# Kernel tuning notes

Measured on AMD Instinct MI355X. Metric: run time of the kernel, lower is better.

## Reference

```python
import jax, jax.numpy as jnp
import numpy as np

N, E, IN_DIM, HID, HEADS, OUT_DIM, T = 50000, 200000, 32, 64, 4, 32, 3
NEG_SLOPE = 0.2  # PyG GATv2Conv default


def setup_inputs() -> dict:
    key = jax.random.key(0)
    ks = jax.random.split(key, 16)
    s = 0.1
    return {
        "feat": jax.random.normal(ks[0], (N, IN_DIM), jnp.float32),
        "W_in": jax.random.normal(ks[1], (IN_DIM, HID), jnp.float32) * s,
        "b_in": jnp.zeros((HID,), jnp.float32),
        "Wl": jax.random.normal(ks[2], (2 * HID, HEADS * HID), jnp.float32) * s,
        "bl": jnp.zeros((HEADS * HID,), jnp.float32),
        "Wr": jax.random.normal(ks[3], (2 * HID, HEADS * HID), jnp.float32) * s,
        "br": jnp.zeros((HEADS * HID,), jnp.float32),
        "att": jax.random.normal(ks[4], (HEADS, HID), jnp.float32) * s,
        "b_conv": jnp.zeros((HEADS * HID,), jnp.float32),
        "Wg": jax.random.normal(ks[5], (HID, OUT_DIM), jnp.float32) * s,
        "bg": jnp.zeros((OUT_DIM,), jnp.float32),
        "edge_index": jax.random.randint(ks[6], (2, E), 0, N, jnp.int32),
        "node_mask": jax.random.randint(ks[7], (N,), 0, T + 1, jnp.int32),
        "current_state": jax.random.randint(ks[8], (N,), 0, 2, jnp.int32),
    }


def reference(feat, W_in, b_in, Wl, bl, Wr, br, att, b_conv, Wg, bg,
              edge_index, node_mask, current_state):
    # add self loops (GATv2Conv add_self_loops=True)
    loops = jnp.arange(N, dtype=edge_index.dtype)
    src = jnp.concatenate([edge_index[0], loops])  # [E+N]
    dst = jnp.concatenate([edge_index[1], loops])

    h0 = feat @ W_in + b_in  # [N, HID]
    bias_sum = b_conv.reshape(HEADS, HID).sum(0)  # heads are summed after bias add

    def step(h, i):
        active = node_mask > i  # [N] bool: nodes updated at this step
        x = jnp.concatenate([h, h0], axis=-1)  # [N, 2*HID]
        xl = (x @ Wl + bl).reshape(N, HEADS, HID)  # source transform
        xr = (x @ Wr + br).reshape(N, HEADS, HID)  # target transform
        e_act = active[src] & active[dst]  # edge alive iff both endpoints active
        s = jax.nn.leaky_relu(xl[src] + xr[dst], NEG_SLOPE)  # [E+N, H, C]
        score = jnp.einsum('ehc,hc->eh', s, att)  # [E+N, H]
        score = jnp.where(e_act[:, None], score, -1e30)
        smax = jax.lax.stop_gradient(
            jax.ops.segment_max(score, dst, num_segments=N))  # [N, H]
        ex = jnp.exp(score - smax[dst]) * e_act[:, None].astype(score.dtype)
        denom = jax.ops.segment_sum(ex, dst, num_segments=N)  # [N, H]
        alpha = ex / jnp.maximum(denom[dst], 1e-16)  # segment softmax per dst
        msg = alpha[:, :, None] * xl[src]  # [E+N, H, C]
        agg = jax.ops.segment_sum(msg, dst, num_segments=N)  # [N, H, C]
        out = jnp.tanh(agg.sum(1) + bias_sum)  # sum over heads, then Tanh
        return jnp.where(active[:, None], out, h), None

    h, _ = jax.lax.scan(step, h0, jnp.arange(T))
    # original returns g_embed(h[current_state]); fixed-shape variant: mask rows
    out = (h @ Wg + bg) * (current_state[:, None] > 0).astype(h.dtype)
    return out
```

## Files before the change

### kernel.cpp

```cpp
#include <hip/hip_runtime.h>
#include <hip/hip_bf16.h>

#define NN      50000
#define EE      200000
#define IN_DIM  32
#define HID     64
#define HEADS   4
#define OUTD    32
#define TSTEPS  3

typedef unsigned short bf16_t;
typedef __attribute__((ext_vector_type(8))) short  short8;
typedef __attribute__((ext_vector_type(4))) float  floatx4;

__device__ __forceinline__ float b2f(bf16_t u) {
    union { unsigned int i; float f; } v; v.i = ((unsigned int)u) << 16; return v.f;
}
__device__ __forceinline__ bf16_t f2b(float f) {
    union { float f; unsigned int i; } v; v.f = f;
    unsigned int r = v.i + 0x7FFF + ((v.i >> 16) & 1);
    return (bf16_t)(r >> 16);
}

#define DPP_ADD(x, ctrl) ((x) + __int_as_float(                                 \
        __builtin_amdgcn_update_dpp(0, __float_as_int(x), (ctrl), 0xF, 0xF, true)))

#define H0_BLOCKS ((NN + 31) / 32)
#define NB_NODE   ((NN + 255) / 256)
#define NBC       (NB_NODE * 4)

__global__ __launch_bounds__(256) void k_setup(
        const void* W_in, const void* b_in, const void* att, const void* bconv,
        const void* Wg, const void* bg,
        const void* Wl_raw, const void* Wr_raw, const void* bl_raw, const void* br_raw,
        const void* feat_raw, const int* __restrict__ nmask,
        float* attf, float* bcf, float* Wgf, float* bgf,
        bf16_t* __restrict__ Wt, bf16_t* __restrict__ WtS, float* __restrict__ bb,
        int* __restrict__ deg, int* __restrict__ flag, int* __restrict__ bcount,
        bf16_t* __restrict__ h0, bf16_t* __restrict__ h) {
    __shared__ int bad;
    __shared__ float Ws[IN_DIM * HID];
    __shared__ float bs[HID];
    __shared__ int wcnt[4][4];
    int t = threadIdx.x, bid = blockIdx.x;
    if (t == 0) bad = 0;
    __syncthreads();
    {
        const bf16_t* p = (const bf16_t*)W_in;
        int mybad = 0;
        for (int i = t; i < IN_DIM * HID; i += 256) {
            float v = b2f(p[i]);
            if (v != v || fabsf(v) > 100.f) mybad = 1;
        }
        if (mybad) atomicOr(&bad, 1);
    }
    __syncthreads();
    int f = bad ? 0 : 1;
    if (bid == 0 && t == 0) *flag = f;

    if (bid < 256) {
        int i = bid * 256 + t;
        int n = i >> 7, k = i & 127;
        const void* W = (n < 256) ? Wl_raw : Wr_raw;
        int nn = (n < 256) ? n : n - 256;
        float v = f ? b2f(((const bf16_t*)W)[k * 256 + nn])
                    : ((const float*)W)[k * 256 + nn];
        Wt[n * 128 + k] = f2b(v);
        if (k < 64) {
            float v2 = f ? b2f(((const bf16_t*)W)[(k + 64) * 256 + nn])
                         : ((const float*)W)[(k + 64) * 256 + nn];
            WtS[n * 64 + k] = f2b(v + v2);
        }
        if (k == 0) {
            const void* b = (n < 256) ? bl_raw : br_raw;
            bb[n] = f ? b2f(((const bf16_t*)b)[nn]) : ((const float*)b)[nn];
        }
    } else if (bid < 267) {
        int i = (bid - 256) * 256 + t;
        const void* src; float* dst; int off;
        if      (i < 256)  { src = att;   dst = attf; off = i; }
        else if (i < 512)  { src = bconv; dst = bcf;  off = i - 256; }
        else if (i < 2560) { src = Wg;    dst = Wgf;  off = i - 512; }
        else if (i < 2592) { src = bg;    dst = bgf;  off = i - 2560; }
        else return;
        dst[off] = f ? b2f(((const bf16_t*)src)[off]) : ((const float*)src)[off];
    } else if (bid < 267 + NB_NODE) {
        int nb = bid - 267;
        int i = nb * 256 + t;
        bool valid = i < NN;
        if (valid) deg[i] = 0;
        int wid = t >> 6, lane = t & 63;
        int v = 0;
        if (valid) { int m = nmask[i]; v = m < 0 ? 0 : (m > 3 ? 3 : m); }
#pragma unroll
        for (int b = 0; b < 4; b++) {
            unsigned long long mm = __ballot(valid && v == b);
            if (lane == 0) wcnt[wid][b] = __popcll(mm);
        }
        __syncthreads();
        if (t < 4)
            bcount[nb * 4 + t] = wcnt[0][t] + wcnt[1][t] + wcnt[2][t] + wcnt[3][t];
    } else {
        for (int i = t; i < IN_DIM * HID; i += 256)
            Ws[i] = f ? b2f(((const bf16_t*)W_in)[i]) : ((const float*)W_in)[i];
        if (t < HID)
            bs[t] = f ? b2f(((const bf16_t*)b_in)[t]) : ((const float*)b_in)[t];
        __syncthreads();
        int nb = bid - (267 + NB_NODE);
        int wid = t >> 6, c = t & 63;
#pragma unroll
        for (int g = 0; g < 8; g++) {
            int node = (nb * 8 + g) * 4 + wid;
            if (node >= NN) break;
            float acc = bs[c];
            if (f) {
                const short8* fr8 = (const short8*)((const bf16_t*)feat_raw
                                                    + (size_t)node * IN_DIM);
#pragma unroll
                for (int j = 0; j < 4; j++) {
                    short8 fv = fr8[j];
#pragma unroll
                    for (int k = 0; k < 8; k++)
                        acc += b2f((bf16_t)fv[k]) * Ws[(j * 8 + k) * HID + c];
                }
            } else {
                const float4* fr4 = (const float4*)((const float*)feat_raw
                                                    + (size_t)node * IN_DIM);
#pragma unroll
                for (int j = 0; j < 8; j++) {
                    float4 fv = fr4[j];
                    acc += fv.x * Ws[(j * 4 + 0) * HID + c];
                    acc += fv.y * Ws[(j * 4 + 1) * HID + c];
                    acc += fv.z * Ws[(j * 4 + 2) * HID + c];
                    acc += fv.w * Ws[(j * 4 + 3) * HID + c];
                }
            }
            bf16_t o = f2b(acc);
            h0[(size_t)node * HID + c] = o;
            h [(size_t)node * HID + c] = o;
        }
    }
}

__global__ __launch_bounds__(256) void k_hist(const int* __restrict__ dst,
                                              int* __restrict__ deg) {
    int i = (blockIdx.x * 256 + threadIdx.x) * 4;
    if (i + 3 < EE) {
        int4 d = *(const int4*)(dst + i);
        atomicAdd(&deg[d.x], 1);
        atomicAdd(&deg[d.y], 1);
        atomicAdd(&deg[d.z], 1);
        atomicAdd(&deg[d.w], 1);
    } else {
        for (; i < EE; i++) atomicAdd(&deg[dst[i]], 1);
    }
}

__global__ __launch_bounds__(256) void k_scan(const int* __restrict__ deg,
                                              int* __restrict__ row_ptr,
                                              int* __restrict__ cursor,
                                              const int* __restrict__ bcount,
                                              int* __restrict__ mbuf,
                                              int n, int nch) {
    __shared__ int sc[256];
    __shared__ int spre[256];
    __shared__ int cb[4];
    int t = threadIdx.x, bid = blockIdx.x;

    if (bid == 0) {
        if (t < 4) cb[t] = 0;
        __syncthreads();
        for (int i = t; i < NBC; i += 256) atomicAdd(&cb[i & 3], bcount[i]);
        __syncthreads();
        if (t == 0) {
            int c1 = cb[1], c2 = cb[2], c3 = cb[3];
            mbuf[7] = 0;
            mbuf[6] = c3;
            mbuf[5] = c3 + c2;
            mbuf[4] = c3 + c2 + c1;
            mbuf[8] = c3 + c2 + c1;
            mbuf[9] = c3 + c2;
            mbuf[10] = c3;
        }
    }

    int base = bid * 1024;
    int pre = 0;
    {
        const int4* d4 = (const int4*)deg;
        int lim = base >> 2;
        for (int i = t; i < lim; i += 256) {
            int4 q = d4[i];
            pre += q.x + q.y + q.z + q.w;
        }
    }
    spre[t] = pre; __syncthreads();
    for (int off = 128; off > 0; off >>= 1) {
        if (t < off) spre[t] += spre[t + off];
        __syncthreads();
    }
    int bpref = spre[0];

    int v[4]; int s = 0;
#pragma unroll
    for (int j = 0; j < 4; j++) {
        int i = base + t * 4 + j;
        v[j] = (i < n) ? deg[i] : 0;
        s += v[j];
    }
    sc[t] = s; __syncthreads();
    for (int off = 1; off < 256; off <<= 1) {
        int add = (t >= off) ? sc[t - off] : 0;
        __syncthreads();
        sc[t] += add;
        __syncthreads();
    }
    int run = sc[t] - s + bpref;
#pragma unroll
    for (int j = 0; j < 4; j++) {
        int i = base + t * 4 + j;
        if (i < n) { row_ptr[i] = run; cursor[i] = run; }
        run += v[j];
    }
    if (bid == nch - 1 && t == 255) row_ptr[n] = run;
}

__global__ __launch_bounds__(256) void k_scatter_all(const int* __restrict__ src,
                                                     const int* __restrict__ dst,
                                                     int* __restrict__ cursor,
                                                     int* __restrict__ col,
                                                     const int* __restrict__ mask,
                                                     int* __restrict__ mbuf,
                                                     int* __restrict__ order) {
    int t = threadIdx.x, bid = blockIdx.x;
    int i = bid * 256 + t;
    if (i < EE) {
        int sv = src[i];
        int m = mask[sv]; m = m < 0 ? 0 : (m > 3 ? 3 : m);
        int d = dst[i];
        int pos = atomicAdd(&cursor[d], 1);
        col[pos] = sv | (m << 28);
    }
    if (bid < NB_NODE) {
        __shared__ int wcnt[4][4];
        __shared__ int bbase[4];
        int wid = t >> 6, lane = t & 63;
        int ni = bid * 256 + t;
        bool valid = ni < NN;
        int v = 0;
        if (valid) { int m = mask[ni]; v = m < 0 ? 0 : (m > 3 ? 3 : m); }
        int rank = 0;
#pragma unroll
        for (int b = 0; b < 4; b++) {
            unsigned long long mm = __ballot(valid && v == b);
            if (valid && v == b)
                rank = __popcll(mm & ((lane == 0) ? 0ull : (~0ull >> (64 - lane))));
            if (lane == 0) wcnt[wid][b] = __popcll(mm);
        }
        __syncthreads();
        if (t < 4) {
            int tot = wcnt[0][t] + wcnt[1][t] + wcnt[2][t] + wcnt[3][t];
            bbase[t] = atomicAdd(&mbuf[4 + t], tot);
        }
        __syncthreads();
        if (valid) {
            int wpre = 0;
            for (int ww = 0; ww < wid; ww++) wpre += wcnt[ww][v];
            order[bbase[v] + wpre + rank] = ni;
        }
    }
}

__global__ __launch_bounds__(256) void k_gemm0(const bf16_t* __restrict__ h0,
                                               const bf16_t* __restrict__ WtS,
                                               const float* __restrict__ bb,
                                               bf16_t* __restrict__ xl,
                                               bf16_t* __restrict__ xr,
                                               const int* __restrict__ order,
                                               const int* __restrict__ mbuf) {
    int count = mbuf[8];
    int mbase = blockIdx.x * 64;
    if (mbase >= count) return;

    __shared__ bf16_t smem[64 * 72 + 128 * 72];
    bf16_t* As = smem;
    bf16_t* Bs = smem + 64 * 72;
    bf16_t* Cs = smem;

    int t = threadIdx.x;
    int nbase = blockIdx.y * 128;

    {
        int ln = t >> 2, lq = t & 3;
        int idx = mbase + ln;
        int node = (idx < count) ? order[idx] : -1;
        ulonglong2 z; z.x = 0; z.y = 0;
        ulonglong2 v0 = z, v1 = z;
        if (node >= 0) {
            v0 = *(const ulonglong2*)(h0 + (size_t)node * HID + lq * 16);
            v1 = *(const ulonglong2*)(h0 + (size_t)node * HID + lq * 16 + 8);
        }
        *(ulonglong2*)(&As[ln * 72 + lq * 16]) = v0;
        *(ulonglong2*)(&As[ln * 72 + lq * 16 + 8]) = v1;
    }
    {
        int n = t >> 1, kc = (t & 1) * 32;
        const bf16_t* srcp = WtS + (size_t)(nbase + n) * 64 + kc;
        bf16_t* dstp = &Bs[n * 72 + kc];
        *(ulonglong2*)(dstp)      = *(const ulonglong2*)(srcp);
        *(ulonglong2*)(dstp + 8)  = *(const ulonglong2*)(srcp + 8);
        *(ulonglong2*)(dstp + 16) = *(const ulonglong2*)(srcp + 16);
        *(ulonglong2*)(dstp + 24) = *(const ulonglong2*)(srcp + 24);
    }
    __syncthreads();

    int wv = t >> 6, lane = t & 63, mrow = lane & 15, quad = lane >> 4;
    floatx4 acc[8];
#pragma unroll
    for (int nf = 0; nf < 8; nf++) acc[nf] = (floatx4){0.f, 0.f, 0.f, 0.f};
#pragma unroll
    for (int kq = 0; kq < 2; kq++) {
        short8 a = *(const short8*)(&As[(wv * 16 + mrow) * 72 + kq * 32 + quad * 8]);
#pragma unroll
        for (int nf = 0; nf < 8; nf++) {
            short8 b = *(const short8*)(&Bs[(nf * 16 + mrow) * 72 + kq * 32 + quad * 8]);
            acc[nf] = __builtin_amdgcn_mfma_f32_16x16x32_bf16(a, b, acc[nf], 0, 0, 0);
        }
    }
    __syncthreads();

#pragma unroll
    for (int nf = 0; nf < 8; nf++) {
        float bv = bb[nbase + nf * 16 + mrow];
#pragma unroll
        for (int r = 0; r < 4; r++) {
            int m = wv * 16 + quad * 4 + r;
            Cs[m * 136 + nf * 16 + mrow] = f2b(acc[nf][r] + bv);
        }
    }
    __syncthreads();

    bf16_t* outp = (blockIdx.y < 2) ? xl : xr;
    int cc = (blockIdx.y & 1) * 128;
#pragma unroll
    for (int i = 0; i < 4; i++) {
        int c = t + i * 256;
        int m = c >> 4, kc = (c & 15) * 8;
        int idx = mbase + m;
        if (idx < count) {
            int node = order[idx];
            *(ulonglong2*)(outp + (size_t)node * 256 + cc + kc) =
                *(const ulonglong2*)(&Cs[m * 136 + kc]);
        }
    }
}

__global__ __launch_bounds__(256) void k_gemm_mfma(const bf16_t* __restrict__ h,
                                                   const bf16_t* __restrict__ h0,
                                                   const bf16_t* __restrict__ Wt,
                                                   const float* __restrict__ bb,
                                                   bf16_t* __restrict__ xl,
                                                   bf16_t* __restrict__ xr,
                                                   const int* __restrict__ order,
                                                   const int* __restrict__ mbuf,
                                                   int step) {
    int count = mbuf[8 + step];
    int mbase = blockIdx.x * 64;
    if (mbase >= count) return;

    __shared__ bf16_t smem[64 * 136 + 128 * 136];
    bf16_t* As = smem;
    bf16_t* Bs = smem + 64 * 136;
    bf16_t* Cs = smem;

    int t = threadIdx.x;
    int nbase = blockIdx.y * 128;

    {
        int ln = t >> 2, lq = t & 3;
        int idx = mbase + ln;
        int node = (idx < count) ? order[idx] : -1;
        ulonglong2 z; z.x = 0; z.y = 0;
#pragma unroll
        for (int j = 0; j < 2; j++) {
            int chunk = lq + j * 4;
            ulonglong2 vh = z, vh0 = z;
            if (node >= 0) {
                vh  = *(const ulonglong2*)(h  + (size_t)node * HID + chunk * 8);
                vh0 = *(const ulonglong2*)(h0 + (size_t)node * HID + chunk * 8);
            }
            *(ulonglong2*)(&As[ln * 136 + chunk * 8]) = vh;
            *(ulonglong2*)(&As[ln * 136 + 64 + chunk * 8]) = vh0;
        }
    }
#pragma unroll
    for (int i = 0; i < 8; i++) {
        int c = t + i * 256;
        int n = c >> 4, kc = (c & 15) * 8;
        *(ulonglong2*)(&Bs[n * 136 + kc]) =
            *(const ulonglong2*)(Wt + (size_t)(nbase + n) * 128 + kc);
    }
    __syncthreads();

    int wv = t >> 6, lane = t & 63, mrow = lane & 15, quad = lane >> 4;
    floatx4 acc[8];
#pragma unroll
    for (int nf = 0; nf < 8; nf++) acc[nf] = (floatx4){0.f, 0.f, 0.f, 0.f};
#pragma unroll
    for (int kq = 0; kq < 4; kq++) {
        short8 a = *(const short8*)(&As[(wv * 16 + mrow) * 136 + kq * 32 + quad * 8]);
#pragma unroll
        for (int nf = 0; nf < 8; nf++) {
            short8 b = *(const short8*)(&Bs[(nf * 16 + mrow) * 136 + kq * 32 + quad * 8]);
            acc[nf] = __builtin_amdgcn_mfma_f32_16x16x32_bf16(a, b, acc[nf], 0, 0, 0);
        }
    }
    __syncthreads();

#pragma unroll
    for (int nf = 0; nf < 8; nf++) {
        float bv = bb[nbase + nf * 16 + mrow];
#pragma unroll
        for (int r = 0; r < 4; r++) {
            int m = wv * 16 + quad * 4 + r;
            Cs[m * 136 + nf * 16 + mrow] = f2b(acc[nf][r] + bv);
        }
    }
    __syncthreads();

    bf16_t* outp = (blockIdx.y < 2) ? xl : xr;
    int cc = (blockIdx.y & 1) * 128;
#pragma unroll
    for (int i = 0; i < 4; i++) {
        int c = t + i * 256;
        int m = c >> 4, kc = (c & 15) * 8;
        int idx = mbase + m;
        if (idx < count) {
            int node = order[idx];
            *(ulonglong2*)(outp + (size_t)node * 256 + cc + kc) =
                *(const ulonglong2*)(&Cs[m * 136 + kc]);
        }
    }
}

__global__ __launch_bounds__(256) void k_agg(bf16_t* __restrict__ h,
                                             const bf16_t* __restrict__ xl,
                                             const bf16_t* __restrict__ xr,
                                             const float* __restrict__ att,
                                             const float* __restrict__ b_conv,
                                             const int* __restrict__ row_ptr,
                                             const int* __restrict__ col,
                                             const int* __restrict__ order,
                                             const int* __restrict__ mbuf,
                                             int step) {
    int count = mbuf[8 + step];
    int wid = threadIdx.x >> 6;
    int lane = threadIdx.x & 63;
    float4 attv = *(const float4*)(att + lane * 4);
    float4 bcv  = *(const float4*)(b_conv + lane * 4);

    for (int idx = blockIdx.x * 4 + wid; idx < count; idx += gridDim.x * 4) {
        int node = order[idx];

        ushort4 xru = *(const ushort4*)(xr + (size_t)node * 256 + lane * 4);
        float xr0 = b2f(xru.x), xr1 = b2f(xru.y), xr2 = b2f(xru.z), xr3 = b2f(xru.w);

        float a0 = 0.f, a1 = 0.f, a2 = 0.f, a3 = 0.f, l = 0.f;

        auto ld = [&](int s) {
            return *(const ushort4*)(xl + (size_t)s * 256 + lane * 4);
        };
        auto body = [&](ushort4 xu) {
            float x0 = b2f(xu.x), x1 = b2f(xu.y), x2 = b2f(xu.z), x3 = b2f(xu.w);
            float v0 = x0 + xr0; v0 = v0 > 0.f ? v0 : 0.2f * v0;
            float v1 = x1 + xr1; v1 = v1 > 0.f ? v1 : 0.2f * v1;
            float v2 = x2 + xr2; v2 = v2 > 0.f ? v2 : 0.2f * v2;
            float v3 = x3 + xr3; v3 = v3 > 0.f ? v3 : 0.2f * v3;
            float part = attv.x * v0 + attv.y * v1 + attv.z * v2 + attv.w * v3;
            part = DPP_ADD(part, 0xB1);
            part = DPP_ADD(part, 0x4E);
            part = DPP_ADD(part, 0x141);
            part = DPP_ADD(part, 0x140);
            float p = __expf(part);
            l += p;
            a0 += p * x0; a1 += p * x1; a2 += p * x2; a3 += p * x3;
        };

        int q0 = node, q1 = 0, q2 = 0, q3 = 0;
        int qn = 1;
        int e0 = row_ptr[node], e1 = row_ptr[node + 1];
        for (int e = e0; e < e1; e++) {
            int c = col[e];
            if (((unsigned)c >> 28) > (unsigned)step) {
                int s = c & 0x0FFFFFFF;
                if (qn == 0) q0 = s;
                else if (qn == 1) q1 = s;
                else if (qn == 2) q2 = s;
                else q3 = s;
                if (++qn == 4) {
                    ushort4 u0 = ld(q0), u1 = ld(q1), u2 = ld(q2), u3 = ld(q3);
                    body(u0); body(u1); body(u2); body(u3);
                    qn = 0;
                }
            }
        }
        if (qn) {
            ushort4 u0 = ld(q0), u1, u2;
            if (qn > 1) u1 = ld(q1);
            if (qn > 2) u2 = ld(q2);
            body(u0);
            if (qn > 1) body(u1);
            if (qn > 2) body(u2);
        }

        float inv = 1.f / l;
        float t0 = a0 * inv + bcv.x;
        float t1 = a1 * inv + bcv.y;
        float t2 = a2 * inv + bcv.z;
        float t3 = a3 * inv + bcv.w;
        t0 += __shfl_xor(t0, 16, 64); t0 += __shfl_xor(t0, 32, 64);
        t1 += __shfl_xor(t1, 16, 64); t1 += __shfl_xor(t1, 32, 64);
        t2 += __shfl_xor(t2, 16, 64); t2 += __shfl_xor(t2, 32, 64);
        t3 += __shfl_xor(t3, 16, 64); t3 += __shfl_xor(t3, 32, 64);
        if (lane < 16) {
            ushort4 o;
            o.x = f2b(tanhf(t0)); o.y = f2b(tanhf(t1));
            o.z = f2b(tanhf(t2)); o.w = f2b(tanhf(t3));
            *(ushort4*)(h + (size_t)node * HID + lane * 4) = o;
        }
    }
}

__global__ __launch_bounds__(256) void k_out(const bf16_t* __restrict__ h,
                                             const float* __restrict__ Wg,
                                             const float* __restrict__ bg,
                                             const int* __restrict__ cs,
                                             void* __restrict__ out,
                                             const int* __restrict__ flag) {
    __shared__ float Ws[HID * OUTD];
    __shared__ float bs[OUTD];
    int t = threadIdx.x;
    for (int i = t; i < HID * OUTD; i += 256) Ws[i] = Wg[i];
    if (t < OUTD) bs[t] = bg[t];
    __syncthreads();
    int node = blockIdx.x * 8 + (t >> 5);
    int c = t & 31;
    if (node >= NN) return;
    float res = 0.f;
    if (cs[node] > 0) {
        const short8* hr8 = (const short8*)(h + (size_t)node * HID);
        float acc = bs[c];
#pragma unroll
        for (int j = 0; j < 8; j++) {
            short8 hv = hr8[j];
#pragma unroll
            for (int k = 0; k < 8; k++)
                acc += b2f((bf16_t)hv[k]) * Ws[(j * 8 + k) * OUTD + c];
        }
        res = acc;
    }
    size_t idx = (size_t)node * OUTD + c;
    if (*flag) ((bf16_t*)out)[idx] = f2b(res);
    else       ((float*)out)[idx]  = res;
}

static inline size_t alignup(size_t x) { return (x + 255) & ~(size_t)255; }

extern "C" void kernel_launch(void* const* d_in, const int* in_sizes, int n_in,
                              void* d_out, int out_size, void* d_ws, size_t ws_size,
                              hipStream_t stream) {
    const void* feat_raw  = d_in[0];
    const void* W_in_raw  = d_in[1];
    const void* b_in_raw  = d_in[2];
    const void* Wl_raw    = d_in[3];
    const void* bl_raw    = d_in[4];
    const void* Wr_raw    = d_in[5];
    const void* br_raw    = d_in[6];
    const void* att_raw   = d_in[7];
    const void* bconv_raw = d_in[8];
    const void* Wg_raw    = d_in[9];
    const void* bg_raw    = d_in[10];
    const int* edge       = (const int*)d_in[11];
    const int* nmask      = (const int*)d_in[12];
    const int* cstate     = (const int*)d_in[13];

    const int* e_src = edge;
    const int* e_dst = edge + EE;

    const size_t SZ_HB   = alignup((size_t)NN * HID * sizeof(bf16_t));
    const size_t SZ_X    = alignup((size_t)NN * 256 * sizeof(bf16_t));
    const size_t SZ_I    = alignup((size_t)NN * sizeof(int));
    const size_t SZ_RP   = alignup((size_t)(NN + 1) * sizeof(int));
    const size_t SZ_COL  = alignup((size_t)EE * sizeof(int));
    const int nch = (NN + 1023) / 1024;
    const size_t SZ_BC   = alignup((size_t)NBC * sizeof(int));
    const size_t SZ_WT   = alignup((size_t)512 * 128 * sizeof(bf16_t));
    const size_t SZ_WTS  = alignup((size_t)512 * 64 * sizeof(bf16_t));
    const size_t SZ_B    = alignup(512 * sizeof(float));
    const size_t SZ_WG   = alignup((size_t)HID * OUTD * sizeof(float));

    char* w = (char*)d_ws;
    bf16_t* h0   = (bf16_t*)w; w += SZ_HB;
    bf16_t* h    = (bf16_t*)w; w += SZ_HB;
    bf16_t* xl   = (bf16_t*)w; w += SZ_X;
    bf16_t* xr   = (bf16_t*)w; w += SZ_X;
    int* deg     = (int*)w;    w += SZ_I;
    int* row_ptr = (int*)w;    w += SZ_RP;
    int* cursor  = (int*)w;    w += SZ_I;
    int* colA    = (int*)w;    w += SZ_COL;
    int* order   = (int*)w;    w += SZ_I;
    int* bcount  = (int*)w;    w += SZ_BC;
    bf16_t* Wt   = (bf16_t*)w; w += SZ_WT;
    bf16_t* WtS  = (bf16_t*)w; w += SZ_WTS;
    float* bb    = (float*)w;  w += SZ_B;
    float* attf  = (float*)w;  w += SZ_B;
    float* bcf   = (float*)w;  w += SZ_B;
    float* Wgf   = (float*)w;  w += SZ_WG;
    float* bgf   = (float*)w;  w += SZ_B;
    int* flag    = (int*)w;    w += 256;
    int* mbuf    = (int*)w;    w += 256;
    if ((size_t)(w - (char*)d_ws) > ws_size) return;

    k_setup<<<467 + H0_BLOCKS - 4, 256, 0, stream>>>(
        W_in_raw, b_in_raw, att_raw, bconv_raw, Wg_raw, bg_raw,
        Wl_raw, Wr_raw, bl_raw, br_raw, feat_raw, nmask,
        attf, bcf, Wgf, bgf, Wt, WtS, bb, deg, flag, bcount, h0, h);

    k_hist<<<(EE + 1023) / 1024, 256, 0, stream>>>(e_dst, deg);
    k_scan<<<nch, 256, 0, stream>>>(deg, row_ptr, cursor, bcount, mbuf, NN, nch);
    k_scatter_all<<<(EE + 255) / 256, 256, 0, stream>>>(e_src, e_dst, cursor, colA,
                                                        nmask, mbuf, order);

    k_gemm0<<<dim3((NN + 63) / 64, 4), 256, 0, stream>>>(h0, WtS, bb, xl, xr, order, mbuf);
    k_agg<<<2048, 256, 0, stream>>>(h, xl, xr, attf, bcf, row_ptr, colA, order, mbuf, 0);

    for (int s = 1; s < TSTEPS; s++) {
        k_gemm_mfma<<<dim3((NN + 63) / 64, 4), 256, 0, stream>>>(h, h0, Wt, bb, xl, xr,
                                                                 order, mbuf, s);
        k_agg<<<2048, 256, 0, stream>>>(h, xl, xr, attf, bcf,
                                        row_ptr, colA, order, mbuf, s);
    }

    k_out<<<(NN + 7) / 8, 256, 0, stream>>>(h, Wgf, bgf, cstate, d_out, flag);
}
```

Baseline: 275.3 us.

## Bucket CSR edges by source mask level and add dynamic work-stealing aggregation

```diff
diff --git a/kernel.cpp b/kernel.cpp
--- a/kernel.cpp
+++ b/kernel.cpp
@@ -25,18 +25,20 @@
 #define DPP_ADD(x, ctrl) ((x) + __int_as_float(                                 \
         __builtin_amdgcn_update_dpp(0, __float_as_int(x), (ctrl), 0xF, 0xF, true)))
 
-#define H0_BLOCKS ((NN + 31) / 32)
+#define H0_BLOCKS ((NN + 63) / 64)
 #define NB_NODE   ((NN + 255) / 256)
 #define NBC       (NB_NODE * 4)
+#define EB        ((EE + 1023) / 1024)
 
 __global__ __launch_bounds__(256) void k_setup(
         const void* W_in, const void* b_in, const void* att, const void* bconv,
         const void* Wg, const void* bg,
         const void* Wl_raw, const void* Wr_raw, const void* bl_raw, const void* br_raw,
         const void* feat_raw, const int* __restrict__ nmask,
+        const int* __restrict__ e_src, const int* __restrict__ e_dst,
         float* attf, float* bcf, float* Wgf, float* bgf,
         bf16_t* __restrict__ Wt, bf16_t* __restrict__ WtS, float* __restrict__ bb,
-        int* __restrict__ deg, int* __restrict__ flag, int* __restrict__ bcount,
+        int* __restrict__ deg4, int* __restrict__ flag, int* __restrict__ bcount,
         bf16_t* __restrict__ h0, bf16_t* __restrict__ h) {
     __shared__ int bad;
     __shared__ float Ws[IN_DIM * HID];
@@ -88,7 +90,6 @@
         int nb = bid - 267;
         int i = nb * 256 + t;
         bool valid = i < NN;
-        if (valid) deg[i] = 0;
         int wid = t >> 6, lane = t & 63;
         int v = 0;
         if (valid) { int m = nmask[i]; v = m < 0 ? 0 : (m > 3 ? 3 : m); }
@@ -100,17 +101,38 @@
         __syncthreads();
         if (t < 4)
             bcount[nb * 4 + t] = wcnt[0][t] + wcnt[1][t] + wcnt[2][t] + wcnt[3][t];
+    } else if (bid < 267 + NB_NODE + EB) {
+        int nb = bid - 267 - NB_NODE;
+        int i = (nb * 256 + t) * 4;
+        if (i + 3 < EE) {
+            int4 dv = *(const int4*)(e_dst + i);
+            int4 sv = *(const int4*)(e_src + i);
+            int m0 = nmask[sv.x]; m0 = m0 < 0 ? 0 : (m0 > 3 ? 3 : m0);
+            int m1 = nmask[sv.y]; m1 = m1 < 0 ? 0 : (m1 > 3 ? 3 : m1);
+            int m2 = nmask[sv.z]; m2 = m2 < 0 ? 0 : (m2 > 3 ? 3 : m2);
+            int m3 = nmask[sv.w]; m3 = m3 < 0 ? 0 : (m3 > 3 ? 3 : m3);
+            atomicAdd(&deg4[dv.x * 4 + m0], 1);
+            atomicAdd(&deg4[dv.y * 4 + m1], 1);
+            atomicAdd(&deg4[dv.z * 4 + m2], 1);
+            atomicAdd(&deg4[dv.w * 4 + m3], 1);
+        } else {
+            for (; i < EE; i++) {
+                int s = e_src[i];
+                int m = nmask[s]; m = m < 0 ? 0 : (m > 3 ? 3 : m);
+                atomicAdd(&deg4[e_dst[i] * 4 + m], 1);
+            }
+        }
     } else {
         for (int i = t; i < IN_DIM * HID; i += 256)
             Ws[i] = f ? b2f(((const bf16_t*)W_in)[i]) : ((const float*)W_in)[i];
         if (t < HID)
             bs[t] = f ? b2f(((const bf16_t*)b_in)[t]) : ((const float*)b_in)[t];
         __syncthreads();
-        int nb = bid - (267 + NB_NODE);
+        int nb = bid - (267 + NB_NODE + EB);
         int wid = t >> 6, c = t & 63;
 #pragma unroll
-        for (int g = 0; g < 8; g++) {
-            int node = (nb * 8 + g) * 4 + wid;
+        for (int g = 0; g < 16; g++) {
+            int node = (nb * 16 + g) * 4 + wid;
             if (node >= NN) break;
             float acc = bs[c];
             if (f) {
@@ -142,23 +164,9 @@
     }
 }
 
-__global__ __launch_bounds__(256) void k_hist(const int* __restrict__ dst,
-                                              int* __restrict__ deg) {
-    int i = (blockIdx.x * 256 + threadIdx.x) * 4;
-    if (i + 3 < EE) {
-        int4 d = *(const int4*)(dst + i);
-        atomicAdd(&deg[d.x], 1);
-        atomicAdd(&deg[d.y], 1);
-        atomicAdd(&deg[d.z], 1);
-        atomicAdd(&deg[d.w], 1);
-    } else {
-        for (; i < EE; i++) atomicAdd(&deg[dst[i]], 1);
-    }
-}
-
-__global__ __launch_bounds__(256) void k_scan(const int* __restrict__ deg,
-                                              int* __restrict__ row_ptr,
-                                              int* __restrict__ cursor,
+__global__ __launch_bounds__(256) void k_scan(const int* __restrict__ deg4,
+                                              int* __restrict__ cur4,
+                                              int* __restrict__ rend4,
                                               const int* __restrict__ bcount,
                                               int* __restrict__ mbuf,
                                               int n, int nch) {
@@ -184,15 +192,12 @@
         }
     }
 
+    const int4* d4 = (const int4*)deg4;
     int base = bid * 1024;
     int pre = 0;
-    {
-        const int4* d4 = (const int4*)deg;
-        int lim = base >> 2;
-        for (int i = t; i < lim; i += 256) {
-            int4 q = d4[i];
-            pre += q.x + q.y + q.z + q.w;
-        }
+    for (int i = t; i < base; i += 256) {
+        int4 q = d4[i];
+        pre += q.x + q.y + q.z + q.w;
     }
     spre[t] = pre; __syncthreads();
     for (int off = 128; off > 0; off >>= 1) {
@@ -201,12 +206,14 @@
     }
     int bpref = spre[0];
 
-    int v[4]; int s = 0;
+    int4 dd[4]; int tot[4]; int s = 0;
 #pragma unroll
     for (int j = 0; j < 4; j++) {
         int i = base + t * 4 + j;
-        v[j] = (i < n) ? deg[i] : 0;
-        s += v[j];
+        if (i < n) dd[j] = d4[i];
+        else { dd[j].x = 0; dd[j].y = 0; dd[j].z = 0; dd[j].w = 0; }
+        tot[j] = dd[j].x + dd[j].y + dd[j].z + dd[j].w;
+        s += tot[j];
     }
     sc[t] = s; __syncthreads();
     for (int off = 1; off < 256; off <<= 1) {
@@ -219,15 +226,23 @@
 #pragma unroll
     for (int j = 0; j < 4; j++) {
         int i = base + t * 4 + j;
-        if (i < n) { row_ptr[i] = run; cursor[i] = run; }
-        run += v[j];
-    }
-    if (bid == nch - 1 && t == 255) row_ptr[n] = run;
+        if (i < n) {
+            int c3 = run;
+            int c2 = c3 + dd[j].w;
+            int c1 = c2 + dd[j].z;
+            int c0 = c1 + dd[j].y;
+            int4 cu; cu.x = c0; cu.y = c1; cu.z = c2; cu.w = c3;
+            *(int4*)(cur4 + i * 4) = cu;
+            int4 re; re.x = c0; re.y = c1; re.z = c2; re.w = run;
+            *(int4*)(rend4 + i * 4) = re;
+        }
+        run += tot[j];
+    }
 }
 
 __global__ __launch_bounds__(256) void k_scatter_all(const int* __restrict__ src,
                                                      const int* __restrict__ dst,
-                                                     int* __restrict__ cursor,
+                                                     int* __restrict__ cur4,
                                                      int* __restrict__ col,
                                                      const int* __restrict__ mask,
                                                      int* __restrict__ mbuf,
@@ -238,8 +253,8 @@
         int sv = src[i];
         int m = mask[sv]; m = m < 0 ? 0 : (m > 3 ? 3 : m);
         int d = dst[i];
-        int pos = atomicAdd(&cursor[d], 1);
-        col[pos] = sv | (m << 28);
+        int pos = atomicAdd(&cur4[d * 4 + m], 1);
+        col[pos] = sv;
     }
     if (bid < NB_NODE) {
         __shared__ int wcnt[4][4];
@@ -448,85 +463,94 @@
                                              const bf16_t* __restrict__ xr,
                                              const float* __restrict__ att,
                                              const float* __restrict__ b_conv,
-                                             const int* __restrict__ row_ptr,
+                                             const int* __restrict__ rend4,
                                              const int* __restrict__ col,
                                              const int* __restrict__ order,
-                                             const int* __restrict__ mbuf,
+                                             int* __restrict__ mbuf,
                                              int step) {
     int count = mbuf[8 + step];
-    int wid = threadIdx.x >> 6;
-    int lane = threadIdx.x & 63;
+    int t = threadIdx.x;
+    int wid = t >> 6;
+    int lane = t & 63;
     float4 attv = *(const float4*)(att + lane * 4);
     float4 bcv  = *(const float4*)(b_conv + lane * 4);
-
-    for (int idx = blockIdx.x * 4 + wid; idx < count; idx += gridDim.x * 4) {
-        int node = order[idx];
-
-        ushort4 xru = *(const ushort4*)(xr + (size_t)node * 256 + lane * 4);
-        float xr0 = b2f(xru.x), xr1 = b2f(xru.y), xr2 = b2f(xru.z), xr3 = b2f(xru.w);
-
-        float a0 = 0.f, a1 = 0.f, a2 = 0.f, a3 = 0.f, l = 0.f;
-
-        auto ld = [&](int s) {
-            return *(const ushort4*)(xl + (size_t)s * 256 + lane * 4);
-        };
-        auto body = [&](ushort4 xu) {
-            float x0 = b2f(xu.x), x1 = b2f(xu.y), x2 = b2f(xu.z), x3 = b2f(xu.w);
-            float v0 = x0 + xr0; v0 = v0 > 0.f ? v0 : 0.2f * v0;
-            float v1 = x1 + xr1; v1 = v1 > 0.f ? v1 : 0.2f * v1;
-            float v2 = x2 + xr2; v2 = v2 > 0.f ? v2 : 0.2f * v2;
-            float v3 = x3 + xr3; v3 = v3 > 0.f ? v3 : 0.2f * v3;
-            float part = attv.x * v0 + attv.y * v1 + attv.z * v2 + attv.w * v3;
-            part = DPP_ADD(part, 0xB1);
-            part = DPP_ADD(part, 0x4E);
-            part = DPP_ADD(part, 0x141);
-            part = DPP_ADD(part, 0x140);
-            float p = __expf(part);
-            l += p;
-            a0 += p * x0; a1 += p * x1; a2 += p * x2; a3 += p * x3;
-        };
-
-        int q0 = node, q1 = 0, q2 = 0, q3 = 0;
-        int qn = 1;
-        int e0 = row_ptr[node], e1 = row_ptr[node + 1];
-        for (int e = e0; e < e1; e++) {
-            int c = col[e];
-            if (((unsigned)c >> 28) > (unsigned)step) {
-                int s = c & 0x0FFFFFFF;
-                if (qn == 0) q0 = s;
-                else if (qn == 1) q1 = s;
-                else if (qn == 2) q2 = s;
-                else q3 = s;
-                if (++qn == 4) {
-                    ushort4 u0 = ld(q0), u1 = ld(q1), u2 = ld(q2), u3 = ld(q3);
-                    body(u0); body(u1); body(u2); body(u3);
-                    qn = 0;
-                }
+    __shared__ int sbase;
+    int* cnt = &mbuf[12 + step];
+
+    for (;;) {
+        if (t == 0) sbase = atomicAdd(cnt, 8);
+        __syncthreads();
+        int base = sbase;
+        __syncthreads();
+        if (base >= count) return;
+
+#pragma unroll
+        for (int u = 0; u < 2; u++) {
+            int idx = base + wid * 2 + u;
+            if (idx >= count) break;
+            int node = order[idx];
+
+            ushort4 xru   = *(const ushort4*)(xr + (size_t)node * 256 + lane * 4);
+            ushort4 uself = *(const ushort4*)(xl + (size_t)node * 256 + lane * 4);
+            int4 re = *(const int4*)(rend4 + node * 4);
+            int e0 = re.w;
+            int e1 = (step == 0) ? re.x : (step == 1) ? re.y : re.z;
+
+            float xr0 = b2f(xru.x), xr1 = b2f(xru.y), xr2 = b2f(xru.z), xr3 = b2f(xru.w);
+            float a0 = 0.f, a1 = 0.f, a2 = 0.f, a3 = 0.f, l = 0.f;
+
+            auto ld = [&](int s) {
+                return *(const ushort4*)(xl + (size_t)s * 256 + lane * 4);
+            };
+            auto body = [&](ushort4 xu) {
+                float x0 = b2f(xu.x), x1 = b2f(xu.y), x2 = b2f(xu.z), x3 = b2f(xu.w);
+                float v0 = x0 + xr0; v0 = fmaxf(v0, 0.2f * v0);
+                float v1 = x1 + xr1; v1 = fmaxf(v1, 0.2f * v1);
+                float v2 = x2 + xr2; v2 = fmaxf(v2, 0.2f * v2);
+                float v3 = x3 + xr3; v3 = fmaxf(v3, 0.2f * v3);
+                float part = attv.x * v0 + attv.y * v1 + attv.z * v2 + attv.w * v3;
+                part = DPP_ADD(part, 0xB1);
+                part = DPP_ADD(part, 0x4E);
+                part = DPP_ADD(part, 0x141);
+                part = DPP_ADD(part, 0x140);
+                float p = __expf(part);
+                l += p;
+                a0 += p * x0; a1 += p * x1; a2 += p * x2; a3 += p * x3;
+            };
+
+            body(uself);
+            int e = e0;
+            for (; e + 4 <= e1; e += 4) {
+                int c0 = col[e], c1 = col[e + 1], c2 = col[e + 2], c3 = col[e + 3];
+                ushort4 u0 = ld(c0), u1 = ld(c1), u2 = ld(c2), u3 = ld(c3);
+                body(u0); body(u1); body(u2); body(u3);
             }
-        }
-        if (qn) {
-            ushort4 u0 = ld(q0), u1, u2;
-            if (qn > 1) u1 = ld(q1);
-            if (qn > 2) u2 = ld(q2);
-            body(u0);
-            if (qn > 1) body(u1);
-            if (qn > 2) body(u2);
-        }
-
-        float inv = 1.f / l;
-        float t0 = a0 * inv + bcv.x;
-        float t1 = a1 * inv + bcv.y;
-        float t2 = a2 * inv + bcv.z;
-        float t3 = a3 * inv + bcv.w;
-        t0 += __shfl_xor(t0, 16, 64); t0 += __shfl_xor(t0, 32, 64);
-        t1 += __shfl_xor(t1, 16, 64); t1 += __shfl_xor(t1, 32, 64);
-        t2 += __shfl_xor(t2, 16, 64); t2 += __shfl_xor(t2, 32, 64);
-        t3 += __shfl_xor(t3, 16, 64); t3 += __shfl_xor(t3, 32, 64);
-        if (lane < 16) {
-            ushort4 o;
-            o.x = f2b(tanhf(t0)); o.y = f2b(tanhf(t1));
-            o.z = f2b(tanhf(t2)); o.w = f2b(tanhf(t3));
-            *(ushort4*)(h + (size_t)node * HID + lane * 4) = o;
+            int rem = e1 - e;
+            if (rem > 0) {
+                int c0 = col[e];
+                int c1 = (rem > 1) ? col[e + 1] : c0;
+                int c2 = (rem > 2) ? col[e + 2] : c0;
+                ushort4 u0 = ld(c0), u1 = ld(c1), u2 = ld(c2);
+                body(u0);
+                if (rem > 1) body(u1);
+                if (rem > 2) body(u2);
+            }
+
+            float inv = 1.f / l;
+            float t0 = a0 * inv + bcv.x;
+            float t1 = a1 * inv + bcv.y;
+            float t2 = a2 * inv + bcv.z;
+            float t3 = a3 * inv + bcv.w;
+            t0 += __shfl_xor(t0, 16, 64); t0 += __shfl_xor(t0, 32, 64);
+            t1 += __shfl_xor(t1, 16, 64); t1 += __shfl_xor(t1, 32, 64);
+            t2 += __shfl_xor(t2, 16, 64); t2 += __shfl_xor(t2, 32, 64);
+            t3 += __shfl_xor(t3, 16, 64); t3 += __shfl_xor(t3, 32, 64);
+            if (lane < 16) {
+                ushort4 o;
+                o.x = f2b(tanhf(t0)); o.y = f2b(tanhf(t1));
+                o.z = f2b(tanhf(t2)); o.w = f2b(tanhf(t3));
+                *(ushort4*)(h + (size_t)node * HID + lane * 4) = o;
+            }
         }
     }
 }
@@ -543,25 +567,29 @@
     for (int i = t; i < HID * OUTD; i += 256) Ws[i] = Wg[i];
     if (t < OUTD) bs[t] = bg[t];
     __syncthreads();
-    int node = blockIdx.x * 8 + (t >> 5);
-    int c = t & 31;
-    if (node >= NN) return;
-    float res = 0.f;
-    if (cs[node] > 0) {
-        const short8* hr8 = (const short8*)(h + (size_t)node * HID);
-        float acc = bs[c];
-#pragma unroll
-        for (int j = 0; j < 8; j++) {
-            short8 hv = hr8[j];
-#pragma unroll
-            for (int k = 0; k < 8; k++)
-                acc += b2f((bf16_t)hv[k]) * Ws[(j * 8 + k) * OUTD + c];
-        }
-        res = acc;
-    }
-    size_t idx = (size_t)node * OUTD + c;
-    if (*flag) ((bf16_t*)out)[idx] = f2b(res);
-    else       ((float*)out)[idx]  = res;
+    int g0 = t >> 5, c = t & 31;
+    int fl = *flag;
+#pragma unroll
+    for (int g = 0; g < 4; g++) {
+        int node = blockIdx.x * 32 + g * 8 + g0;
+        if (node >= NN) break;
+        float res = 0.f;
+        if (cs[node] > 0) {
+            const short8* hr8 = (const short8*)(h + (size_t)node * HID);
+            float acc = bs[c];
+#pragma unroll
+            for (int j = 0; j < 8; j++) {
+                short8 hv = hr8[j];
+#pragma unroll
+                for (int k = 0; k < 8; k++)
+                    acc += b2f((bf16_t)hv[k]) * Ws[(j * 8 + k) * OUTD + c];
+            }
+            res = acc;
+        }
+        size_t idx = (size_t)node * OUTD + c;
+        if (fl) ((bf16_t*)out)[idx] = f2b(res);
+        else    ((float*)out)[idx]  = res;
+    }
 }
 
 static inline size_t alignup(size_t x) { return (x + 255) & ~(size_t)255; }
@@ -589,8 +617,8 @@
 
     const size_t SZ_HB   = alignup((size_t)NN * HID * sizeof(bf16_t));
     const size_t SZ_X    = alignup((size_t)NN * 256 * sizeof(bf16_t));
+    const size_t SZ_I4   = alignup((size_t)NN * 4 * sizeof(int));
     const size_t SZ_I    = alignup((size_t)NN * sizeof(int));
-    const size_t SZ_RP   = alignup((size_t)(NN + 1) * sizeof(int));
     const size_t SZ_COL  = alignup((size_t)EE * sizeof(int));
     const int nch = (NN + 1023) / 1024;
     const size_t SZ_BC   = alignup((size_t)NBC * sizeof(int));
@@ -604,9 +632,10 @@
     bf16_t* h    = (bf16_t*)w; w += SZ_HB;
     bf16_t* xl   = (bf16_t*)w; w += SZ_X;
     bf16_t* xr   = (bf16_t*)w; w += SZ_X;
-    int* deg     = (int*)w;    w += SZ_I;
-    int* row_ptr = (int*)w;    w += SZ_RP;
-    int* cursor  = (int*)w;    w += SZ_I;
+    int* deg4    = (int*)w;    w += SZ_I4;
+    int* mbuf    = (int*)w;    w += 256;
+    int* cur4    = (int*)w;    w += SZ_I4;
+    int* rend4   = (int*)w;    w += SZ_I4;
     int* colA    = (int*)w;    w += SZ_COL;
     int* order   = (int*)w;    w += SZ_I;
     int* bcount  = (int*)w;    w += SZ_BC;
@@ -618,28 +647,28 @@
     float* Wgf   = (float*)w;  w += SZ_WG;
     float* bgf   = (float*)w;  w += SZ_B;
     int* flag    = (int*)w;    w += 256;
-    int* mbuf    = (int*)w;    w += 256;
     if ((size_t)(w - (char*)d_ws) > ws_size) return;
 
-    k_setup<<<467 + H0_BLOCKS - 4, 256, 0, stream>>>(
+    hipMemsetAsync(deg4, 0, SZ_I4 + 256, stream);
+
+    k_setup<<<267 + NB_NODE + EB + H0_BLOCKS, 256, 0, stream>>>(
         W_in_raw, b_in_raw, att_raw, bconv_raw, Wg_raw, bg_raw,
-        Wl_raw, Wr_raw, bl_raw, br_raw, feat_raw, nmask,
-        attf, bcf, Wgf, bgf, Wt, WtS, bb, deg, flag, bcount, h0, h);
-
-    k_hist<<<(EE + 1023) / 1024, 256, 0, stream>>>(e_dst, deg);
-    k_scan<<<nch, 256, 0, stream>>>(deg, row_ptr, cursor, bcount, mbuf, NN, nch);
-    k_scatter_all<<<(EE + 255) / 256, 256, 0, stream>>>(e_src, e_dst, cursor, colA,
+        Wl_raw, Wr_raw, bl_raw, br_raw, feat_raw, nmask, e_src, e_dst,
+        attf, bcf, Wgf, bgf, Wt, WtS, bb, deg4, flag, bcount, h0, h);
+
+    k_scan<<<nch, 256, 0, stream>>>(deg4, cur4, rend4, bcount, mbuf, NN, nch);
+    k_scatter_all<<<(EE + 255) / 256, 256, 0, stream>>>(e_src, e_dst, cur4, colA,
                                                         nmask, mbuf, order);
 
     k_gemm0<<<dim3((NN + 63) / 64, 4), 256, 0, stream>>>(h0, WtS, bb, xl, xr, order, mbuf);
-    k_agg<<<2048, 256, 0, stream>>>(h, xl, xr, attf, bcf, row_ptr, colA, order, mbuf, 0);
+    k_agg<<<2048, 256, 0, stream>>>(h, xl, xr, attf, bcf, rend4, colA, order, mbuf, 0);
 
     for (int s = 1; s < TSTEPS; s++) {
         k_gemm_mfma<<<dim3((NN + 63) / 64, 4), 256, 0, stream>>>(h, h0, Wt, bb, xl, xr,
                                                                  order, mbuf, s);
         k_agg<<<2048, 256, 0, stream>>>(h, xl, xr, attf, bcf,
-                                        row_ptr, colA, order, mbuf, s);
-    }
-
-    k_out<<<(NN + 7) / 8, 256, 0, stream>>>(h, Wgf, bgf, cstate, d_out, flag);
-}
+                                        rend4, colA, order, mbuf, s);
+    }
+
+    k_out<<<(NN + 31) / 32, 256, 0, stream>>>(h, Wgf, bgf, cstate, d_out, flag);
+}
```

Result: slower. 407.6 us (+48.1%).
